# Optimization experiments

Hardware: AMD Instinct MI355X
Metric: run time of the kernel (lower is better)

The kernel has to match this reference:

```python
import jax, jax.numpy as jnp
import numpy as np

B, N, F_IN, F_OUT = 8, 2048, 64, 64
ALPHA = 0.2
NEG = -9e15


def setup_inputs() -> dict:
    key = jax.random.key(0)
    k1, k2, k3, k4 = jax.random.split(key, 4)
    h = jax.random.normal(k1, (B, N, F_IN), dtype=jnp.float32)
    adj = jax.random.randint(k2, (N, N), 0, 2).astype(jnp.float32)
    W = jax.random.normal(k3, (F_OUT, F_IN), dtype=jnp.float32) * 0.05
    a = jax.random.normal(k4, (2 * F_OUT,), dtype=jnp.float32) * 0.05
    return {"h": h, "adj": adj, "W": W, "a": a}


def reference(h, adj, W, a):
    # Wh = h @ W^T  : [B, N, F_OUT]
    Wh = jnp.einsum("bnf,of->bno", h, W)
    # a([Wh_i, Wh_j]) decomposes exactly into a1.Wh_i + a2.Wh_j
    e1 = Wh @ a[:F_OUT]          # [B, N] contribution of source node i
    e2 = Wh @ a[F_OUT:]          # [B, N] contribution of target node j
    e = jax.nn.leaky_relu(e1[:, :, None] + e2[:, None, :], negative_slope=ALPHA)
    att = jnp.where(adj[None, :, :] > 0, e, NEG)
    att = jax.nn.softmax(att, axis=-1)   # [B, N, N]
    h_prime = jnp.einsum("bij,bjo->bio", att, Wh)
    return jax.nn.elu(h_prime)
```

## Files before the change

### kernel.cpp

```cpp
#include <hip/hip_runtime.h>
#include <hip/hip_bf16.h>
#include <math.h>


#define NN 2048
#define BB 8

typedef __attribute__((ext_vector_type(8))) short s8v;
typedef __attribute__((ext_vector_type(4))) float f4v;
typedef __attribute__((ext_vector_type(16))) float f16v;
typedef __attribute__((ext_vector_type(4))) unsigned u4v;
typedef __attribute__((ext_vector_type(2))) unsigned long long u64v2;

static __device__ __forceinline__ unsigned pk_bf16(float lo, float hi) {
  __hip_bfloat162 t = __float22bfloat162_rn(float2{lo, hi});
  return *(unsigned*)&t;
}
static __device__ __forceinline__ unsigned short bf16rne(float x) {
  union { float f; unsigned u; } c; c.f = x;
  unsigned r = c.u + 0x7FFFu + ((c.u >> 16) & 1u);
  return (unsigned short)(r >> 16);
}

__global__ __launch_bounds__(256, 2) void k_pre(
    const float* __restrict__ adj, const float* __restrict__ h,
    const float* __restrict__ W, const float* __restrict__ a,
    unsigned long long* __restrict__ adjq, unsigned short* __restrict__ whswz,
    float2* __restrict__ e1pn, unsigned* __restrict__ e2pk) {
  const int t = threadIdx.x, lane = t & 63, w = t >> 6;

  if (blockIdx.x >= 512) {
    const int bid = blockIdx.x - 512;
    const int row = bid * 2 + (w >> 1);
    const int half = w & 1;
    const float* ar = adj + (size_t)row * NN + half * 1024;
    unsigned long long* aq = adjq + row * 32 + half * 16;
    #pragma unroll
    for (int it = 0; it < 16; ++it) {
      unsigned long long m = __ballot(ar[it * 64 + lane] > 0.f);
      if (lane == 0) aq[it] = m;
    }
    return;
  }

  __shared__ __align__(16) float hs[32][68];
  const int rowBase = blockIdx.x * 32;
  const int b = rowBase >> 11, n0 = rowBase & (NN - 1);

  float wr[64];
  #pragma unroll
  for (int k = 0; k < 16; ++k)
    *(f4v*)&wr[k * 4] = *(const f4v*)&W[lane * 64 + k * 4];

  #pragma unroll
  for (int qq = 0; qq < 2; ++qq) {
    const int idx = t + 256 * qq;
    const int r = idx >> 4, c = (idx & 15) * 4;
    *(f4v*)&hs[r][c] = *(const f4v*)&h[(size_t)(rowBase + r) * 64 + c];
  }
  const float a1v = a[lane], a2v = a[64 + lane];
  __syncthreads();

  const int r0 = w * 8;
  float acc[8];
  #pragma unroll
  for (int rr = 0; rr < 8; ++rr) acc[rr] = 0.f;
  #pragma unroll
  for (int f4i = 0; f4i < 16; ++f4i) {
    f4v hv[8];
    #pragma unroll
    for (int rr = 0; rr < 8; ++rr)
      hv[rr] = *(const f4v*)&hs[r0 + rr][f4i * 4];
    #pragma unroll
    for (int x = 0; x < 4; ++x) {
      const float wv = wr[f4i * 4 + x];
      #pragma unroll
      for (int rr = 0; rr < 8; ++rr) acc[rr] = fmaf(hv[rr][x], wv, acc[rr]);
    }
  }

  {
    union { s8v v; unsigned u[4]; } cv;
    cv.u[0] = pk_bf16(acc[0], acc[1]);
    cv.u[1] = pk_bf16(acc[2], acc[3]);
    cv.u[2] = pk_bf16(acc[4], acc[5]);
    cv.u[3] = pk_bf16(acc[6], acc[7]);
    const int jc = (n0 + w * 8) >> 4;
    const int oh = lane >> 5;
    const int lp = ((w & 1) << 5) + (lane & 31);
    unsigned short* dst = whswz + ((size_t)b << 17) + (jc << 10) + (oh << 9) + (lp << 3);
    *(s8v*)dst = cv.v;
  }

  float s1[8], s2[8];
  #pragma unroll
  for (int rr = 0; rr < 8; ++rr) { s1[rr] = acc[rr] * a1v; s2[rr] = acc[rr] * a2v; }
  #pragma unroll
  for (int m = 1; m < 64; m <<= 1)
    #pragma unroll
    for (int rr = 0; rr < 8; ++rr) {
      s1[rr] += __shfl_xor(s1[rr], m);
      s2[rr] += __shfl_xor(s2[rr], m);
    }
  #pragma unroll
  for (int rr = 0; rr < 8; ++rr) {
    if (lane == 0) {
      e1pn[rowBase + rr + r0] = float2{__expf(s1[rr]), __expf(0.2f * s1[rr])};
      e2pk[rowBase + rr + r0] =
          (unsigned)bf16rne(__expf(s2[rr])) |
          ((unsigned)bf16rne(__expf(0.2f * s2[rr])) << 16);
    }
  }
}

__global__ __launch_bounds__(256, 2) void k_attn(
    const unsigned long long* __restrict__ adjq,
    const unsigned short* __restrict__ whswz,
    const float2* __restrict__ e1png, const unsigned* __restrict__ e2pkg,
    float* __restrict__ out) {
  union SM {
    unsigned e2bf[NN];
    float pc[4][32][68];
  };
  __shared__ __align__(16) SM sm;
  __shared__ float ls[4][32];

  const int t = threadIdx.x, lane = t & 63, w = t >> 6;
  const int m32 = lane & 31, kh = lane >> 5;
  const int g = blockIdx.x;
  const int b = g & 7;
  const int i0 = (g >> 3) << 5;
  const size_t bN = (size_t)b * NN;

  ((u4v*)sm.e2bf)[t] = ((const u4v*)(e2pkg + bN))[t];
  ((u4v*)sm.e2bf)[t + 256] = ((const u4v*)(e2pkg + bN))[t + 256];

  const float2 e1f = e1png[bN + i0 + m32];
  const float E1p = e1f.x, E1n = e1f.y;

  const unsigned long long* arow = adjq + (size_t)(i0 + m32) * 32 + w * 8;
  unsigned long long am[8];
  #pragma unroll
  for (int qq = 0; qq < 4; ++qq)
    *(u64v2*)&am[qq * 2] = *(const u64v2*)(arow + qq * 2);

  const unsigned short* wb = whswz + ((size_t)b << 17) + ((size_t)(w * 32) << 10);

  f16v acc0, acc1;
  #pragma unroll
  for (int r = 0; r < 16; ++r) { acc0[r] = 0.f; acc1[r] = 0.f; }
  float psA = 0.f, psB = 0.f;

  s8v buf[4][2];
  #pragma unroll
  for (int k = 0; k < 4; ++k) {
    buf[k][0] = *(const s8v*)(wb + (k << 10) + (lane << 3));
    buf[k][1] = *(const s8v*)(wb + (k << 10) + 512 + (lane << 3));
  }

  __syncthreads();

  #pragma unroll 4
  for (int k = 0; k < 32; ++k) {
    const int x = k & 3;
    const int eb = ((w * 32 + k) << 4) + (kh << 3);
    const u4v e0 = *(const u4v*)&sm.e2bf[eb];
    const u4v e1 = *(const u4v*)&sm.e2bf[eb + 4];
    const unsigned bits = (unsigned)(am[k >> 2] >> ((k & 3) * 16 + kh * 8)) & 0xffu;
    float p[8];
    #pragma unroll
    for (int e = 0; e < 8; ++e) {
      const unsigned dw = e < 4 ? e0[e] : e1[e - 4];
      const float E2p = __uint_as_float(dw << 16);
      const float E2n = __uint_as_float(dw & 0xffff0000u);
      const float mp = E1p * E2p;
      const float mn = E1n * E2n;
      float pv = mp > 1.f ? mp : mn;
      pv = ((bits >> e) & 1u) ? pv : 0.f;
      p[e] = pv;
    }
    {
      const float s01 = p[0] + p[1], s23 = p[2] + p[3];
      const float s45 = p[4] + p[5], s67 = p[6] + p[7];
      if (k & 1) psB += (s01 + s23) + (s45 + s67);
      else       psA += (s01 + s23) + (s45 + s67);
    }
    s8v af;
    {
      union { s8v v; unsigned u[4]; } cv;
      cv.u[0] = pk_bf16(p[0], p[1]);
      cv.u[1] = pk_bf16(p[2], p[3]);
      cv.u[2] = pk_bf16(p[4], p[5]);
      cv.u[3] = pk_bf16(p[6], p[7]);
      af = cv.v;
    }

    acc0 = __builtin_amdgcn_mfma_f32_32x32x16_bf16(af, buf[x][0], acc0, 0, 0, 0);
    acc1 = __builtin_amdgcn_mfma_f32_32x32x16_bf16(af, buf[x][1], acc1, 0, 0, 0);

    if (k < 28) {
      buf[x][0] = *(const s8v*)(wb + ((k + 4) << 10) + (lane << 3));
      buf[x][1] = *(const s8v*)(wb + ((k + 4) << 10) + 512 + (lane << 3));
    }
  }

  float psum = psA + psB;
  psum += __shfl_xor(psum, 32);
  __syncthreads();
  if (lane < 32) ls[w][lane] = psum;
  #pragma unroll
  for (int r = 0; r < 16; ++r) {
    const int row = (r & 3) + 8 * (r >> 2) + 4 * kh;
    sm.pc[w][row][m32] = acc0[r];
    sm.pc[w][row][32 + m32] = acc1[r];
  }
  __syncthreads();

  const int row = t >> 3, c0 = (t & 7) * 8;
  f4v s0 = *(const f4v*)&sm.pc[0][row][c0];
  f4v s1 = *(const f4v*)&sm.pc[0][row][c0 + 4];
  #pragma unroll
  for (int j = 1; j < 4; ++j) {
    s0 += *(const f4v*)&sm.pc[j][row][c0];
    s1 += *(const f4v*)&sm.pc[j][row][c0 + 4];
  }
  const float rsum = ls[0][row] + ls[1][row] + ls[2][row] + ls[3][row];
  f4v o0, o1;
  #pragma unroll
  for (int xx = 0; xx < 4; ++xx) {
    float v = s0[xx] / rsum;
    o0[xx] = v > 0.f ? v : expm1f(v);
    v = s1[xx] / rsum;
    o1[xx] = v > 0.f ? v : expm1f(v);
  }
  float* op = &out[(bN + i0 + row) * 64 + c0];
  *(f4v*)op = o0;
  *(f4v*)(op + 4) = o1;
}

extern "C" void kernel_launch(void* const* d_in, const int* in_sizes, int n_in,
                              void* d_out, int out_size, void* d_ws, size_t ws_size,
                              hipStream_t stream) {
  (void)in_sizes; (void)n_in; (void)out_size; (void)ws_size;
  const float* h   = (const float*)d_in[0];
  const float* adj = (const float*)d_in[1];
  const float* W   = (const float*)d_in[2];
  const float* a   = (const float*)d_in[3];
  float* outp = (float*)d_out;

  unsigned short* whswz = (unsigned short*)d_ws;
  float2* e1pn = (float2*)((char*)d_ws + (size_t)BB * 64 * NN * 2);
  unsigned* e2pk = (unsigned*)(e1pn + (size_t)BB * NN);
  unsigned long long* adjq = (unsigned long long*)(e2pk + (size_t)BB * NN);

  k_pre<<<1536, 256, 0, stream>>>(adj, h, W, a, adjq, whswz, e1pn, e2pk);
  k_attn<<<512, 256, 0, stream>>>(adjq, whswz, e1pn, e2pk, outp);
}
```

Baseline: 100.4 us.

## Stream Wh tiles through LDS via async global_load_lds triple buffering

Replaces the register-held 4-deep prefetch of Wh B-fragments with direct global-to-LDS asynchronous loads into a three-stage shared-memory ring, using explicit vmcnt waits. The aim is to free VGPRs and hide global latency behind the MFMA and softmax work. The e2 table moves out of the union into its own LDS array, which raises shared-memory use per block and may affect occupancy. It also adds an extra LDS read per step and relies on hand-coded waitcnt values being correct.

```diff
diff --git a/kernel.cpp b/kernel.cpp
--- a/kernel.cpp
+++ b/kernel.cpp
@@ -20,6 +20,12 @@
   union { float f; unsigned u; } c; c.f = x;
   unsigned r = c.u + 0x7FFFu + ((c.u >> 16) & 1u);
   return (unsigned short)(r >> 16);
+}
+static __device__ __forceinline__ void glds16(const unsigned short* g,
+                                              unsigned short* l) {
+  __builtin_amdgcn_global_load_lds(
+      (const __attribute__((address_space(1))) unsigned int*)g,
+      (__attribute__((address_space(3))) unsigned int*)l, 16, 0, 0);
 }
 
 __global__ __launch_bounds__(256, 2) void k_pre(
@@ -119,10 +125,11 @@
     const float2* __restrict__ e1png, const unsigned* __restrict__ e2pkg,
     float* __restrict__ out) {
   union SM {
-    unsigned e2bf[NN];
+    unsigned short sbuf[3][4][1024];
     float pc[4][32][68];
   };
   __shared__ __align__(16) SM sm;
+  __shared__ __align__(16) unsigned e2bf[NN];
   __shared__ float ls[4][32];
 
   const int t = threadIdx.x, lane = t & 63, w = t >> 6;
@@ -132,8 +139,8 @@
   const int i0 = (g >> 3) << 5;
   const size_t bN = (size_t)b * NN;
 
-  ((u4v*)sm.e2bf)[t] = ((const u4v*)(e2pkg + bN))[t];
-  ((u4v*)sm.e2bf)[t + 256] = ((const u4v*)(e2pkg + bN))[t + 256];
+  ((u4v*)e2bf)[t] = ((const u4v*)(e2pkg + bN))[t];
+  ((u4v*)e2bf)[t + 256] = ((const u4v*)(e2pkg + bN))[t + 256];
 
   const float2 e1f = e1png[bN + i0 + m32];
   const float E1p = e1f.x, E1n = e1f.y;
@@ -144,29 +151,36 @@
   for (int qq = 0; qq < 4; ++qq)
     *(u64v2*)&am[qq * 2] = *(const u64v2*)(arow + qq * 2);
 
-  const unsigned short* wb = whswz + ((size_t)b << 17) + ((size_t)(w * 32) << 10);
+  const unsigned short* wbase = whswz + ((size_t)b << 17) + ((size_t)(w * 32) << 10);
 
   f16v acc0, acc1;
   #pragma unroll
   for (int r = 0; r < 16; ++r) { acc0[r] = 0.f; acc1[r] = 0.f; }
   float psA = 0.f, psB = 0.f;
 
-  s8v buf[4][2];
-  #pragma unroll
-  for (int k = 0; k < 4; ++k) {
-    buf[k][0] = *(const s8v*)(wb + (k << 10) + (lane << 3));
-    buf[k][1] = *(const s8v*)(wb + (k << 10) + 512 + (lane << 3));
-  }
-
-  __syncthreads();
-
-  #pragma unroll 4
-  for (int k = 0; k < 32; ++k) {
-    const int x = k & 3;
-    const int eb = ((w * 32 + k) << 4) + (kh << 3);
-    const u4v e0 = *(const u4v*)&sm.e2bf[eb];
-    const u4v e1 = *(const u4v*)&sm.e2bf[eb + 4];
-    const unsigned bits = (unsigned)(am[k >> 2] >> ((k & 3) * 16 + kh * 8)) & 0xffu;
+  #pragma unroll
+  for (int s = 0; s < 2; ++s) {
+    const unsigned short* gp = wbase + (s << 10) + (lane << 3);
+    glds16(gp, &sm.sbuf[s][w][0]);
+    glds16(gp + 512, &sm.sbuf[s][w][512]);
+  }
+
+  __syncthreads();
+
+  #pragma unroll
+  for (int s = 0; s < 32; ++s) {
+    if (s < 31) __builtin_amdgcn_s_waitcnt(0x0F72);
+    else        __builtin_amdgcn_s_waitcnt(0x0F70);
+    __asm__ volatile("" ::: "memory");
+
+    const int r = s % 3;
+    const s8v bf0 = *(const s8v*)&sm.sbuf[r][w][lane << 3];
+    const s8v bf1 = *(const s8v*)&sm.sbuf[r][w][512 + (lane << 3)];
+
+    const int eb = ((w * 32 + s) << 4) + (kh << 3);
+    const u4v e0 = *(const u4v*)&e2bf[eb];
+    const u4v e1 = *(const u4v*)&e2bf[eb + 4];
+    const unsigned bits = (unsigned)(am[s >> 2] >> ((s & 3) * 16 + kh * 8)) & 0xffu;
     float p[8];
     #pragma unroll
     for (int e = 0; e < 8; ++e) {
@@ -182,7 +196,7 @@
     {
       const float s01 = p[0] + p[1], s23 = p[2] + p[3];
       const float s45 = p[4] + p[5], s67 = p[6] + p[7];
-      if (k & 1) psB += (s01 + s23) + (s45 + s67);
+      if (s & 1) psB += (s01 + s23) + (s45 + s67);
       else       psA += (s01 + s23) + (s45 + s67);
     }
     s8v af;
@@ -195,12 +209,15 @@
       af = cv.v;
     }
 
-    acc0 = __builtin_amdgcn_mfma_f32_32x32x16_bf16(af, buf[x][0], acc0, 0, 0, 0);
-    acc1 = __builtin_amdgcn_mfma_f32_32x32x16_bf16(af, buf[x][1], acc1, 0, 0, 0);
-
-    if (k < 28) {
-      buf[x][0] = *(const s8v*)(wb + ((k + 4) << 10) + (lane << 3));
-      buf[x][1] = *(const s8v*)(wb + ((k + 4) << 10) + 512 + (lane << 3));
+    acc0 = __builtin_amdgcn_mfma_f32_32x32x16_bf16(af, bf0, acc0, 0, 0, 0);
+    acc1 = __builtin_amdgcn_mfma_f32_32x32x16_bf16(af, bf1, acc1, 0, 0, 0);
+
+    __asm__ volatile("" ::: "memory");
+    if (s + 2 < 32) {
+      const int rn = (s + 2) % 3;
+      const unsigned short* gp = wbase + ((s + 2) << 10) + (lane << 3);
+      glds16(gp, &sm.sbuf[rn][w][0]);
+      glds16(gp + 512, &sm.sbuf[rn][w][512]);
     }
   }
 
```

Result: no change. 102.0 us (+1.6%).
